# Kernel tuning notes

Hardware: AMD Instinct MI355X
Metric: run time of the kernel (lower is better)

Reference implementation:

```python
import jax, jax.numpy as jnp
import numpy as np

N = 8192       # nodes
IN_F = 512     # in_features
OUT_F = 256    # out_features


def setup_inputs() -> dict:
    key = jax.random.key(0)
    k1, k2, k3, k4 = jax.random.split(key, 4)
    # xavier_uniform-like scales for params
    w_scale = 1.414 * (6.0 / (IN_F + OUT_F)) ** 0.5
    a_scale = 1.414 * (6.0 / (2 * OUT_F + 1)) ** 0.5
    x = jax.random.normal(k1, (N, IN_F), jnp.float32)
    W = jax.random.uniform(k2, (IN_F, OUT_F), jnp.float32, -w_scale, w_scale)
    a = jax.random.uniform(k3, (2 * OUT_F, 1), jnp.float32, -a_scale, a_scale)
    adj = jax.random.randint(k4, (N, N), 0, 2, jnp.int32)
    return {"x": x, "W": W, "a": a, "adj": adj}


def reference(x, W, a, adj):
    # h = x @ W : [N, OUT_F]
    h = x @ W
    f = W.shape[1]
    a1, a2 = a[:f], a[f:]          # each [OUT_F, 1]
    # Original builds a_input[i,j] = concat(h_i, h_j) then matmuls with a.
    # Equivalent decomposition: e[i,j] = h_i . a1 + h_j . a2
    e = (h @ a1) + (h @ a2).T      # [N, N]
    neg = jnp.float32(-9e15)
    attention = jnp.where(adj > 0, e, neg)   # no softmax in the original
    h_prime = attention @ h        # [N, OUT_F]
    return h_prime
```

## Files before the change

kernel.cpp:

```cpp
#include <hip/hip_runtime.h>


#define NEG_BIG (-9000000000000000.0f)

typedef __bf16 bf16x8 __attribute__((ext_vector_type(8)));
typedef float f32x16 __attribute__((ext_vector_type(16)));

static __device__ __forceinline__ unsigned short f2bf(float f) {
  unsigned u = __builtin_bit_cast(unsigned, f);
  u = u + 0x7FFFu + ((u >> 16) & 1u);
  return (unsigned short)(u >> 16);
}
static __device__ __forceinline__ float bfbits2f(unsigned hi16) {
  return __builtin_bit_cast(float, hi16 << 16);
}
static __device__ __forceinline__ unsigned pk2(float a, float b) {
  return (unsigned)f2bf(a) | ((unsigned)f2bf(b) << 16);
}
static __device__ __forceinline__ unsigned m2(int a, int b) {
  return (unsigned)(a + (b << 16)) * 0x3F80u;
}
static __device__ __forceinline__ bf16x8 asbf(int4 q) {
  return __builtin_bit_cast(bf16x8, q);
}
static __device__ __forceinline__ f32x16 mfma(bf16x8 a, int4 b, f32x16 c) {
  return __builtin_amdgcn_mfma_f32_32x32x16_bf16(a, asbf(b), c, 0, 0, 0);
}

__global__ void k1a_wt(const float* __restrict__ W, unsigned short* __restrict__ WT,
                       float* __restrict__ T) {
  const int i = blockIdx.x * 256 + threadIdx.x;
  const int k = i >> 8, n = i & 255;
  WT[n * 512 + k] = f2bf(W[i]);
  if (blockIdx.x == 0) T[threadIdx.x] = 0.f;
}

__global__ __launch_bounds__(256) void k1b_h(const float* __restrict__ x,
    const unsigned short* __restrict__ WT, unsigned short* __restrict__ hP) {
  __shared__ unsigned short XS[64 * 264];
  const int t = threadIdx.x;
  const int mt = blockIdx.x;
  const int m0 = mt << 5;
  const int row = t >> 3, c7 = t & 7;
  const float* xr = x + (size_t)(m0 + row) * 512 + c7 * 4;
  const int gb = c7 >> 1, off = (t & 1) * 4;
#pragma unroll
  for (int j = 0; j < 16; ++j) {
    float4 v = *(const float4*)(xr + 32 * j);
    *(uint2*)&XS[(gb + 4 * j) * 264 + row * 8 + off] =
        make_uint2(pk2(v.x, v.y), pk2(v.z, v.w));
  }
  __syncthreads();
  const int w = t >> 6, l = t & 63, l31 = l & 31, lh = l >> 5;
  f32x16 acc0, acc1;
  for (int i = 0; i < 16; ++i) { acc0[i] = 0.f; acc1[i] = 0.f; }
  const int nt0 = w * 2;
  const unsigned short* w0 = WT + (size_t)(nt0 * 32 + l31) * 512 + lh * 8;
  const unsigned short* w1 = w0 + 32 * 512;
  const char* XB = (const char*)XS + lh * 528 + l31 * 16;
#pragma unroll 4
  for (int ks = 0; ks < 32; ++ks) {
    bf16x8 Af = *(const bf16x8*)(XB + ks * 1056);
    int4 b0 = *(const int4*)(w0 + ks * 16);
    int4 b1 = *(const int4*)(w1 + ks * 16);
    acc0 = mfma(Af, b0, acc0);
    acc1 = mfma(Af, b1, acc1);
  }
#pragma unroll
  for (int reg = 0; reg < 16; ++reg) {
    const int mm = (reg & 3) + 8 * (reg >> 2) + 4 * lh;
    hP[(size_t)mt * 8192 + (nt0 * 32 + l31) * 32 + mm] = f2bf(acc0[reg]);
    hP[(size_t)mt * 8192 + ((nt0 + 1) * 32 + l31) * 32 + mm] = f2bf(acc1[reg]);
  }
}

__global__ __launch_bounds__(256) void k2_colsum(const unsigned short* __restrict__ hP,
                                                 float* __restrict__ T) {
  const int t = threadIdx.x;
  const int b = blockIdx.x;
  const int4* p = (const int4*)(hP + (size_t)b * 8192 + t * 32);
  int4 q0 = p[0], q1 = p[1], q2 = p[2], q3 = p[3];
  float s = 0.f;
  const unsigned* u0 = (const unsigned*)&q0;
  const unsigned* u1 = (const unsigned*)&q1;
  const unsigned* u2 = (const unsigned*)&q2;
  const unsigned* u3 = (const unsigned*)&q3;
#pragma unroll
  for (int i = 0; i < 4; ++i) {
    s += bfbits2f(u0[i] & 0xFFFFu) + bfbits2f(u0[i] >> 16);
    s += bfbits2f(u1[i] & 0xFFFFu) + bfbits2f(u1[i] >> 16);
    s += bfbits2f(u2[i] & 0xFFFFu) + bfbits2f(u2[i] >> 16);
    s += bfbits2f(u3[i] & 0xFFFFu) + bfbits2f(u3[i] >> 16);
  }
  atomicAdd(&T[t], s);
}

__global__ __launch_bounds__(256) void k3_att(const int* __restrict__ adj,
    const unsigned short* __restrict__ hP, const float* __restrict__ T,
    float* __restrict__ out) {
  __shared__ unsigned short S[4][2][1024];
  const int t = threadIdx.x, blk = blockIdx.x;
  const int w = t >> 6, l = t & 63, l31 = l & 31, lh = l >> 5;
  const int r0 = blk * 32;

  const int* aB = adj + (size_t)(r0 + (l >> 3)) * 8192 + (l & 7) * 4;
  const int woff = ((l & 7) >> 1) * 256 + (l >> 3) * 8 + (l & 1) * 4;
  const unsigned short* hB = hP + (size_t)(w * 64 + l31) * 32 + lh * 8;
  const int fr = lh * 512 + l31 * 16;
  unsigned short* const Sw0 = &S[w][0][0];
  unsigned short* const Sw1 = &S[w][1][0];

  f32x16 acc0, acc1;
#pragma unroll
  for (int i = 0; i < 16; ++i) { acc0[i] = 0.f; acc1[i] = 0.f; }

  int4 gA0[4], gA1[4], gA2[4], gA3[4], BvA[4], BvB[4];

#define ALOAD(it, g)                                                        \
  _Pragma("unroll")                                                         \
  for (int q = 0; q < 4; ++q)                                               \
    g[q] = *(const int4*)(aB + (size_t)q * 65536 + (it) * 32);
#define APACK(buf, g)                                                       \
  _Pragma("unroll")                                                         \
  for (int q = 0; q < 4; ++q)                                               \
    *(uint2*)&buf[woff + q * 64] =                                          \
        make_uint2(m2(g[q].x, g[q].y), m2(g[q].z, g[q].w));
#define BLOAD(it, Bv)                                                       \
  {                                                                         \
    const unsigned short* hb = hB + (size_t)(it) * 8192;                    \
    Bv[0] = *(const int4*)(hb);                                             \
    Bv[1] = *(const int4*)(hb + 1024);                                      \
    Bv[2] = *(const int4*)(hb + 16);                                        \
    Bv[3] = *(const int4*)(hb + 1024 + 16);                                 \
  }
#define COMP(buf, Bv)                                                       \
  {                                                                         \
    const char* Ab = (const char*)(buf) + fr;                               \
    bf16x8 A0_ = *(const bf16x8*)(Ab);                                      \
    bf16x8 A1_ = *(const bf16x8*)(Ab + 1024);                               \
    acc0 = mfma(A0_, Bv[0], acc0);                                          \
    acc1 = mfma(A0_, Bv[1], acc1);                                          \
    acc0 = mfma(A1_, Bv[2], acc0);                                          \
    acc1 = mfma(A1_, Bv[3], acc1);                                          \
  }

  ALOAD(0, gA0)
  APACK(Sw0, gA0)
  ALOAD(1, gA1)
  ALOAD(2, gA2)
  BLOAD(0, BvA)

#pragma unroll 1
  for (int it = 0; it < 256; it += 4) {
    BLOAD(it + 1, BvB)
    APACK(Sw1, gA1)
    if (it + 3 < 256) { ALOAD(it + 3, gA3) }
    COMP(Sw0, BvA)

    if (it + 2 < 256) { BLOAD(it + 2, BvA) }
    if (it + 2 < 256) { APACK(Sw0, gA2) }
    if (it + 4 < 256) { ALOAD(it + 4, gA0) }
    COMP(Sw1, BvB)

    if (it + 3 < 256) { BLOAD(it + 3, BvB) }
    if (it + 3 < 256) { APACK(Sw1, gA3) }
    if (it + 5 < 256) { ALOAD(it + 5, gA1) }
    if (it + 2 < 256) { COMP(Sw0, BvA) }

    if (it + 4 < 256) { BLOAD(it + 4, BvA) }
    if (it + 4 < 256) { APACK(Sw0, gA0) }
    if (it + 6 < 256) { ALOAD(it + 6, gA2) }
    if (it + 3 < 256) { COMP(Sw1, BvB) }
  }
#undef ALOAD
#undef APACK
#undef BLOAD
#undef COMP

  const int cb = w * 64 + l31;
  {
    const float tv = T[cb];
#pragma unroll
    for (int reg = 0; reg < 16; ++reg) {
      const int rr = r0 + (reg & 3) + 8 * (reg >> 2) + 4 * lh;
      out[(size_t)rr * 256 + cb] = NEG_BIG * (tv - acc0[reg]);
    }
  }
  {
    const float tv = T[cb + 32];
#pragma unroll
    for (int reg = 0; reg < 16; ++reg) {
      const int rr = r0 + (reg & 3) + 8 * (reg >> 2) + 4 * lh;
      out[(size_t)rr * 256 + cb + 32] = NEG_BIG * (tv - acc1[reg]);
    }
  }
}

extern "C" void kernel_launch(void* const* d_in, const int* in_sizes, int n_in,
                              void* d_out, int out_size, void* d_ws, size_t ws_size,
                              hipStream_t stream) {
  const float* x = (const float*)d_in[0];
  const float* W = (const float*)d_in[1];
  const int* adj = (const int*)d_in[3];
  float* out = (float*)d_out;
  char* ws = (char*)d_ws;
  unsigned short* WT = (unsigned short*)(ws);
  unsigned short* hP = (unsigned short*)(ws + (1 << 20));
  float* T = (float*)(ws + (6 << 20));

  k1a_wt<<<512, 256, 0, stream>>>(W, WT, T);
  k1b_h<<<256, 256, 0, stream>>>(x, WT, hP);
  k2_colsum<<<256, 256, 0, stream>>>(hP, T);
  k3_att<<<256, 256, 0, stream>>>(adj, hP, T, out);
}
```

Baseline: 490.6 us.

## Pre-pack adjacency into bitmask and retile attention matmul with split-K reduction

Adds a pre-pass kernel that compresses the int32 adjacency matrix into a row bitmask using wave ballots. The attention GEMM then reads these compact bits and expands them directly into bf16 MFMA fragments in registers, with no LDS staging. The kernel is also retiled to 64x128 output blocks with split-K across wave pairs, followed by an LDS reduction. The 256MB adjacency read still happens once in the pre-pass, but the main kernel reads far less data; the cost is an extra launch and reduced occupancy (launch bounds 1).

Measured after the change: 442.0 us. -9.9%, faster.

```diff
diff --git a/kernel.cpp b/kernel.cpp
--- a/kernel.cpp
+++ b/kernel.cpp
@@ -17,14 +17,44 @@
 static __device__ __forceinline__ unsigned pk2(float a, float b) {
   return (unsigned)f2bf(a) | ((unsigned)f2bf(b) << 16);
 }
-static __device__ __forceinline__ unsigned m2(int a, int b) {
-  return (unsigned)(a + (b << 16)) * 0x3F80u;
-}
 static __device__ __forceinline__ bf16x8 asbf(int4 q) {
   return __builtin_bit_cast(bf16x8, q);
 }
 static __device__ __forceinline__ f32x16 mfma(bf16x8 a, int4 b, f32x16 c) {
   return __builtin_amdgcn_mfma_f32_32x32x16_bf16(a, asbf(b), c, 0, 0, 0);
+}
+static __device__ __forceinline__ unsigned bp(unsigned da, unsigned db, int p) {
+  return (((da >> p) & 1u) | (((db >> p) & 1u) << 16)) * 0x3F80u;
+}
+static __device__ __forceinline__ bf16x8 mkfrag(unsigned dA, unsigned dB,
+                                                unsigned dC, unsigned dD, int p0) {
+  uint4 u;
+  u.x = bp(dA, dB, p0);
+  u.y = bp(dC, dD, p0);
+  u.z = bp(dA, dB, p0 + 1);
+  u.w = bp(dC, dD, p0 + 1);
+  return __builtin_bit_cast(bf16x8, u);
+}
+
+__global__ __launch_bounds__(256) void k0_bits(const int* __restrict__ adj,
+    unsigned long long* __restrict__ bm) {
+  const int w = threadIdx.x >> 6, l = threadIdx.x & 63;
+  const int row = blockIdx.x * 4 + w;
+  const int4* ar = (const int4*)(adj + (size_t)row * 8192) + l;
+  unsigned long long* br = bm + (size_t)row * 128;
+#pragma unroll 2
+  for (int b = 0; b < 32; ++b) {
+    int4 v = ar[b * 64];
+    unsigned long long b0 = __ballot(v.x > 0);
+    unsigned long long b1 = __ballot(v.y > 0);
+    unsigned long long b2 = __ballot(v.z > 0);
+    unsigned long long b3 = __ballot(v.w > 0);
+    if (l == 0) {
+      ulonglong2* p = (ulonglong2*)(br + (size_t)b * 4);
+      p[0] = make_ulonglong2(b0, b1);
+      p[1] = make_ulonglong2(b2, b3);
+    }
+  }
 }
 
 __global__ void k1a_wt(const float* __restrict__ W, unsigned short* __restrict__ WT,
@@ -95,104 +125,130 @@
   atomicAdd(&T[t], s);
 }
 
-__global__ __launch_bounds__(256) void k3_att(const int* __restrict__ adj,
+__global__ __launch_bounds__(256, 1) void k3_att(
+    const unsigned long long* __restrict__ bm,
     const unsigned short* __restrict__ hP, const float* __restrict__ T,
     float* __restrict__ out) {
-  __shared__ unsigned short S[4][2][1024];
+  __shared__ float red[2][64][64];
   const int t = threadIdx.x, blk = blockIdx.x;
   const int w = t >> 6, l = t & 63, l31 = l & 31, lh = l >> 5;
-  const int r0 = blk * 32;
-
-  const int* aB = adj + (size_t)(r0 + (l >> 3)) * 8192 + (l & 7) * 4;
-  const int woff = ((l & 7) >> 1) * 256 + (l >> 3) * 8 + (l & 1) * 4;
-  const unsigned short* hB = hP + (size_t)(w * 64 + l31) * 32 + lh * 8;
-  const int fr = lh * 512 + l31 * 16;
-  unsigned short* const Sw0 = &S[w][0][0];
-  unsigned short* const Sw1 = &S[w][1][0];
-
-  f32x16 acc0, acc1;
-#pragma unroll
-  for (int i = 0; i < 16; ++i) { acc0[i] = 0.f; acc1[i] = 0.f; }
-
-  int4 gA0[4], gA1[4], gA2[4], gA3[4], BvA[4], BvB[4];
-
-#define ALOAD(it, g)                                                        \
-  _Pragma("unroll")                                                         \
-  for (int q = 0; q < 4; ++q)                                               \
-    g[q] = *(const int4*)(aB + (size_t)q * 65536 + (it) * 32);
-#define APACK(buf, g)                                                       \
-  _Pragma("unroll")                                                         \
-  for (int q = 0; q < 4; ++q)                                               \
-    *(uint2*)&buf[woff + q * 64] =                                          \
-        make_uint2(m2(g[q].x, g[q].y), m2(g[q].z, g[q].w));
-#define BLOAD(it, Bv)                                                       \
+  const int ch = w & 1, s = w >> 1;
+  const int rb = blk >> 1, cb = blk & 1;
+  const int r0 = rb * 64;
+  const int cw0 = cb * 128 + ch * 64;
+  const int lh2 = lh * 2;
+
+  const int4* bmp0 = (const int4*)bm + (size_t)(r0 + l31) * 64 + s * 32;
+  const int4* bmp1 = bmp0 + 32 * 64;
+  const unsigned short* hB = hP + (size_t)(cw0 + l31) * 32 + lh * 8;
+
+  f32x16 acc[2][2];
+#pragma unroll
+  for (int mt = 0; mt < 2; ++mt)
+#pragma unroll
+    for (int nt = 0; nt < 2; ++nt)
+#pragma unroll
+      for (int i = 0; i < 16; ++i) acc[mt][nt][i] = 0.f;
+
+  int4 qA0[2], qA1[2], qB0[2], qB1[2], BvA[4], BvB[4];
+  int jt = s * 128;
+
+#define LOADBM(k, Q0, Q1)                                                   \
+  Q0[0] = bmp0[(k) * 2]; Q0[1] = bmp0[(k) * 2 + 1];                         \
+  Q1[0] = bmp1[(k) * 2]; Q1[1] = bmp1[(k) * 2 + 1];
+
+#define ITER(mm, Q0, Q1, BVC, BVN)                                          \
   {                                                                         \
-    const unsigned short* hb = hB + (size_t)(it) * 8192;                    \
-    Bv[0] = *(const int4*)(hb);                                             \
-    Bv[1] = *(const int4*)(hb + 1024);                                      \
-    Bv[2] = *(const int4*)(hb + 16);                                        \
-    Bv[3] = *(const int4*)(hb + 1024 + 16);                                 \
-  }
-#define COMP(buf, Bv)                                                       \
-  {                                                                         \
-    const char* Ab = (const char*)(buf) + fr;                               \
-    bf16x8 A0_ = *(const bf16x8*)(Ab);                                      \
-    bf16x8 A1_ = *(const bf16x8*)(Ab + 1024);                               \
-    acc0 = mfma(A0_, Bv[0], acc0);                                          \
-    acc1 = mfma(A0_, Bv[1], acc1);                                          \
-    acc0 = mfma(A1_, Bv[2], acc0);                                          \
-    acc1 = mfma(A1_, Bv[3], acc1);                                          \
-  }
-
-  ALOAD(0, gA0)
-  APACK(Sw0, gA0)
-  ALOAD(1, gA1)
-  ALOAD(2, gA2)
-  BLOAD(0, BvA)
+    {                                                                       \
+      const unsigned short* hb_ = hB + (size_t)(jt + 1) * 8192;             \
+      BVN[0] = *(const int4*)(hb_);                                         \
+      BVN[1] = *(const int4*)(hb_ + 16);                                    \
+      BVN[2] = *(const int4*)(hb_ + 1024);                                  \
+      BVN[3] = *(const int4*)(hb_ + 1040);                                  \
+    }                                                                       \
+    const unsigned* q0_ = (const unsigned*)(Q0);                            \
+    const unsigned* q1_ = (const unsigned*)(Q1);                            \
+    const unsigned a0_ = q0_[((mm) >> 2)];                                  \
+    const unsigned b0_ = q0_[2 + ((mm) >> 2)];                              \
+    const unsigned c0_ = q0_[4 + ((mm) >> 2)];                              \
+    const unsigned d0_ = q0_[6 + ((mm) >> 2)];                              \
+    const unsigned a1_ = q1_[((mm) >> 2)];                                  \
+    const unsigned b1_ = q1_[2 + ((mm) >> 2)];                              \
+    const unsigned c1_ = q1_[4 + ((mm) >> 2)];                              \
+    const unsigned d1_ = q1_[6 + ((mm) >> 2)];                              \
+    const int pb_ = 8 * ((mm) & 3) + lh2;                                   \
+    bf16x8 A00 = mkfrag(a0_, b0_, c0_, d0_, pb_);              \
+    bf16x8 A01 = mkfrag(a0_, b0_, c0_, d0_, pb_ + 4);          \
+    bf16x8 A10 = mkfrag(a1_, b1_, c1_, d1_, pb_);              \
+    bf16x8 A11 = mkfrag(a1_, b1_, c1_, d1_, pb_ + 4);          \
+    acc[0][0] = mfma(A00, BVC[0], acc[0][0]);                               \
+    acc[1][0] = mfma(A10, BVC[0], acc[1][0]);                               \
+    acc[0][1] = mfma(A00, BVC[2], acc[0][1]);                               \
+    acc[1][1] = mfma(A10, BVC[2], acc[1][1]);                               \
+    acc[0][0] = mfma(A01, BVC[1], acc[0][0]);                               \
+    acc[1][0] = mfma(A11, BVC[1], acc[1][0]);                               \
+    acc[0][1] = mfma(A01, BVC[3], acc[0][1]);                               \
+    acc[1][1] = mfma(A11, BVC[3], acc[1][1]);                               \
+    ++jt;                                                                   \
+  }
+
+  LOADBM(0, qA0, qA1)
+  {
+    const unsigned short* hb_ = hB + (size_t)jt * 8192;
+    BvA[0] = *(const int4*)(hb_);
+    BvA[1] = *(const int4*)(hb_ + 16);
+    BvA[2] = *(const int4*)(hb_ + 1024);
+    BvA[3] = *(const int4*)(hb_ + 1040);
+  }
 
 #pragma unroll 1
-  for (int it = 0; it < 256; it += 4) {
-    BLOAD(it + 1, BvB)
-    APACK(Sw1, gA1)
-    if (it + 3 < 256) { ALOAD(it + 3, gA3) }
-    COMP(Sw0, BvA)
-
-    if (it + 2 < 256) { BLOAD(it + 2, BvA) }
-    if (it + 2 < 256) { APACK(Sw0, gA2) }
-    if (it + 4 < 256) { ALOAD(it + 4, gA0) }
-    COMP(Sw1, BvB)
-
-    if (it + 3 < 256) { BLOAD(it + 3, BvB) }
-    if (it + 3 < 256) { APACK(Sw1, gA3) }
-    if (it + 5 < 256) { ALOAD(it + 5, gA1) }
-    if (it + 2 < 256) { COMP(Sw0, BvA) }
-
-    if (it + 4 < 256) { BLOAD(it + 4, BvA) }
-    if (it + 4 < 256) { APACK(Sw0, gA0) }
-    if (it + 6 < 256) { ALOAD(it + 6, gA2) }
-    if (it + 3 < 256) { COMP(Sw1, BvB) }
-  }
-#undef ALOAD
-#undef APACK
-#undef BLOAD
-#undef COMP
-
-  const int cb = w * 64 + l31;
-  {
-    const float tv = T[cb];
-#pragma unroll
-    for (int reg = 0; reg < 16; ++reg) {
-      const int rr = r0 + (reg & 3) + 8 * (reg >> 2) + 4 * lh;
-      out[(size_t)rr * 256 + cb] = NEG_BIG * (tv - acc0[reg]);
-    }
-  }
-  {
-    const float tv = T[cb + 32];
-#pragma unroll
-    for (int reg = 0; reg < 16; ++reg) {
-      const int rr = r0 + (reg & 3) + 8 * (reg >> 2) + 4 * lh;
-      out[(size_t)rr * 256 + cb + 32] = NEG_BIG * (tv - acc1[reg]);
-    }
+  for (int bb = 0; bb < 8; ++bb) {
+    LOADBM(bb * 2 + 1, qB0, qB1)
+    ITER(0, qA0, qA1, BvA, BvB)
+    ITER(1, qA0, qA1, BvB, BvA)
+    ITER(2, qA0, qA1, BvA, BvB)
+    ITER(3, qA0, qA1, BvB, BvA)
+    ITER(4, qA0, qA1, BvA, BvB)
+    ITER(5, qA0, qA1, BvB, BvA)
+    ITER(6, qA0, qA1, BvA, BvB)
+    ITER(7, qA0, qA1, BvB, BvA)
+    LOADBM(bb * 2 + 2, qA0, qA1)
+    ITER(0, qB0, qB1, BvA, BvB)
+    ITER(1, qB0, qB1, BvB, BvA)
+    ITER(2, qB0, qB1, BvA, BvB)
+    ITER(3, qB0, qB1, BvB, BvA)
+    ITER(4, qB0, qB1, BvA, BvB)
+    ITER(5, qB0, qB1, BvB, BvA)
+    ITER(6, qB0, qB1, BvA, BvB)
+    ITER(7, qB0, qB1, BvB, BvA)
+  }
+#undef ITER
+#undef LOADBM
+
+  if (s == 1) {
+#pragma unroll
+    for (int mt = 0; mt < 2; ++mt)
+#pragma unroll
+      for (int nt = 0; nt < 2; ++nt)
+#pragma unroll
+        for (int reg = 0; reg < 16; ++reg)
+          red[ch][(mt * 2 + nt) * 16 + reg][l] = acc[mt][nt][reg];
+  }
+  __syncthreads();
+  if (s == 0) {
+#pragma unroll
+    for (int mt = 0; mt < 2; ++mt)
+#pragma unroll
+      for (int nt = 0; nt < 2; ++nt) {
+        const int cc = cw0 + nt * 32 + l31;
+        const float tv = T[cc];
+#pragma unroll
+        for (int reg = 0; reg < 16; ++reg) {
+          const float am = acc[mt][nt][reg] + red[ch][(mt * 2 + nt) * 16 + reg][l];
+          const int rr = r0 + mt * 32 + (reg & 3) + 8 * (reg >> 2) + 4 * lh;
+          out[(size_t)rr * 256 + cc] = NEG_BIG * (tv - am);
+        }
+      }
   }
 }
 
@@ -207,9 +263,11 @@
   unsigned short* WT = (unsigned short*)(ws);
   unsigned short* hP = (unsigned short*)(ws + (1 << 20));
   float* T = (float*)(ws + (6 << 20));
-
+  unsigned long long* bm = (unsigned long long*)(ws + (8 << 20));
+
+  k0_bits<<<2048, 256, 0, stream>>>(adj, bm);
   k1a_wt<<<512, 256, 0, stream>>>(W, WT, T);
   k1b_h<<<256, 256, 0, stream>>>(x, WT, hP);
   k2_colsum<<<256, 256, 0, stream>>>(hP, T);
-  k3_att<<<256, 256, 0, stream>>>(adj, hP, T, out);
-}
+  k3_att<<<256, 256, 0, stream>>>(bm, hP, T, out);
+}
```
